# Kernel optimization log

Measured on AMD Instinct MI355X. Metric: run time of the kernel, lower is better.

## Reference

```python
import jax, jax.numpy as jnp
import numpy as np

N = 50000      # num nodes
E = 1600000    # num edges (before self-loops)
DIN, DH, DOUT = 256, 128, 64


def _gcn_norm(edge_index, num_nodes):
    # Add self-loops, then symmetric normalization 1/sqrt(deg_i * deg_j)
    loop = jnp.arange(num_nodes, dtype=edge_index.dtype)
    src = jnp.concatenate([edge_index[0], loop])  # [E+N]
    dst = jnp.concatenate([edge_index[1], loop])  # [E+N]
    deg = jax.ops.segment_sum(jnp.ones_like(dst, dtype=jnp.float32), dst,
                              num_segments=num_nodes)
    dinv = jnp.where(deg > 0, jax.lax.rsqrt(deg), 0.0)
    norm = dinv[src] * dinv[dst]  # [E+N]
    return src, dst, norm


def _gcn_conv(x, src, dst, norm, W, b, num_nodes):
    h = x @ W                                  # [N, out] dense transform first
    msg = h[src] * norm[:, None]               # gather + scale  [E+N, out]
    out = jax.ops.segment_sum(msg, dst, num_segments=num_nodes)  # scatter-add
    return out + b


def reference(x, edge_index, W1, b1, W2, b2):
    num_nodes = x.shape[0]
    src, dst, norm = _gcn_norm(edge_index, num_nodes)
    h = _gcn_conv(x, src, dst, norm, W1, b1, num_nodes)
    h = jax.nn.relu(h)
    # dropout(p=0.5) is identity in eval mode
    out = _gcn_conv(h, src, dst, norm, W2, b2, num_nodes)
    return out


def setup_inputs() -> dict:
    key = jax.random.key(0)
    ks = jax.random.split(key, 6)
    x = jax.random.normal(ks[0], (N, DIN), dtype=jnp.float32)
    edge_index = jax.random.randint(ks[1], (2, E), 0, N, dtype=jnp.int32)
    W1 = jax.random.normal(ks[2], (DIN, DH), dtype=jnp.float32) * (1.0 / np.sqrt(DIN))
    b1 = jnp.zeros((DH,), dtype=jnp.float32)
    W2 = jax.random.normal(ks[3], (DH, DOUT), dtype=jnp.float32) * (1.0 / np.sqrt(DH))
    b2 = jnp.zeros((DOUT,), dtype=jnp.float32)
    return {"x": x, "edge_index": edge_index, "W1": W1, "b1": b1, "W2": W2, "b2": b2}
```

## Files before the change

kernel.cpp:

```cpp
#include <hip/hip_runtime.h>

#define DIN 256
#define DH  128
#define DOUT 64
#define BSH  7
#define BNODES 128
#define MAXBUK 400
#define NBLK 512

typedef unsigned int  u32;
typedef unsigned short u16;
typedef __attribute__((ext_vector_type(8))) short bf16x8;
typedef __attribute__((ext_vector_type(4))) float f32x4;

__device__ inline u16 f2bf(float f) {
  u32 u = __float_as_uint(f);
  u32 r = u + 0x7FFF + ((u >> 16) & 1);
  return (u16)(r >> 16);
}
__device__ inline float bf2f_lo(u32 packed) { return __uint_as_float(packed << 16); }
__device__ inline float bf2f_hi(u32 packed) { return __uint_as_float(packed & 0xFFFF0000u); }


__global__ __launch_bounds__(256) void hist_kernel(const int* __restrict__ dst,
    int* __restrict__ counts, int E, int nbuk) {
  __shared__ int h[MAXBUK];
  int tid = threadIdx.x, b = blockIdx.x;
  for (int i = tid; i < nbuk; i += 256) h[i] = 0;
  __syncthreads();
  int ech = (E + NBLK - 1) / NBLK;
  int e0 = b * ech, e1 = min(E, e0 + ech);
  for (int e = e0 + tid; e < e1; e += 256)
    atomicAdd(&h[dst[e] >> BSH], 1);
  __syncthreads();
  for (int i = tid; i < nbuk; i += 256) counts[(size_t)i * NBLK + b] = h[i];
}

__global__ __launch_bounds__(256) void col_scan(int* __restrict__ counts,
    int* __restrict__ colsum, int nbuk) {
  __shared__ int sm[256];
  __shared__ int carry;
  int buk = blockIdx.x, t = threadIdx.x;
  if (t == 0) carry = 0;
  __syncthreads();
  int* row = counts + (size_t)buk * NBLK;
  for (int base = 0; base < NBLK; base += 256) {
    int v = row[base + t];
    sm[t] = v;
    __syncthreads();
    for (int d = 1; d < 256; d <<= 1) {
      int a = (t >= d) ? sm[t - d] : 0;
      __syncthreads();
      sm[t] += a;
      __syncthreads();
    }
    int excl = sm[t] - v + carry;
    row[base + t] = excl;
    __syncthreads();
    if (t == 255) carry = excl + v;
    __syncthreads();
  }
  if (t == 0) colsum[buk] = carry;
}

__global__ __launch_bounds__(256) void scan_block(int* partial, int* total_out, int nb, int n) {
  __shared__ int sm[256];
  __shared__ int carry;
  int t = threadIdx.x;
  if (t == 0) carry = 0;
  __syncthreads();
  for (int base = 0; base < nb; base += 256) {
    int g = base + t;
    int v = (g < nb) ? partial[g] : 0;
    sm[t] = v;
    __syncthreads();
    for (int d = 1; d < 256; d <<= 1) {
      int add = (t >= d) ? sm[t - d] : 0;
      __syncthreads();
      sm[t] += add;
      __syncthreads();
    }
    int excl = sm[t] - v + carry;
    if (g < nb) partial[g] = excl;
    __syncthreads();
    if (t == 255) carry = excl + v;
    __syncthreads();
  }
  if (t == 0) total_out[n] = carry;
}

__global__ __launch_bounds__(256) void scatter_kernel(const int* __restrict__ src,
    const int* __restrict__ dst, const int* __restrict__ counts,
    const int* __restrict__ bb, u32* __restrict__ ebuf, int E, int nbuk) {
  __shared__ int cur[MAXBUK];
  int tid = threadIdx.x, b = blockIdx.x;
  for (int i = tid; i < nbuk; i += 256)
    cur[i] = bb[i] + counts[(size_t)i * NBLK + b];
  __syncthreads();
  int ech = (E + NBLK - 1) / NBLK;
  int e0 = b * ech, e1 = min(E, e0 + ech);
  for (int e = e0 + tid; e < e1; e += 256) {
    int d = dst[e];
    int r = atomicAdd(&cur[d >> BSH], 1);
    ebuf[r] = (u32)src[e] | ((u32)(d & (BNODES - 1)) << 16);
  }
}

__global__ __launch_bounds__(256) void bucket_node_count(const u32* __restrict__ ebuf,
    const int* __restrict__ bb, int* __restrict__ cnt, int* __restrict__ bpartial, int N) {
  __shared__ int c[BNODES];
  int b = blockIdx.x, tid = threadIdx.x;
  if (tid < BNODES) c[tid] = 0;
  __syncthreads();
  int e0 = bb[b], e1 = bb[b + 1];
  for (int e = e0 + tid; e < e1; e += 256)
    atomicAdd(&c[ebuf[e] >> 16], 1);
  __syncthreads();
  int node = b * BNODES + tid;
  if (tid < BNODES && node < N) cnt[node] = c[tid];
  if (tid < 64) {
    int s = c[tid] + c[tid + 64];
    #pragma unroll
    for (int o = 32; o > 0; o >>= 1) s += __shfl_down(s, o, 64);
    if (tid == 0) bpartial[b] = s;
  }
}

__global__ __launch_bounds__(256) void scan_chunks(const int* __restrict__ cnt,
    const int* __restrict__ chunkoff, int* __restrict__ rowptr,
    float* __restrict__ dinv, int n) {
  __shared__ int sm[256];
  int t = threadIdx.x, g = blockIdx.x * 256 + t;
  int v = (g < n) ? cnt[g] : 0;
  sm[t] = v;
  __syncthreads();
  for (int d = 1; d < 256; d <<= 1) {
    int add = (t >= d) ? sm[t - d] : 0;
    __syncthreads();
    sm[t] += add;
    __syncthreads();
  }
  if (g < n) {
    rowptr[g] = sm[t] - v + chunkoff[blockIdx.x * 2];
    dinv[g] = rsqrtf((float)(v + 1));
  }
}

__global__ __launch_bounds__(256) void bucket_fill(const u32* __restrict__ ebuf,
    const int* __restrict__ bb, const int* __restrict__ rowptr, u16* __restrict__ csr) {
  __shared__ int c[BNODES];
  int b = blockIdx.x, tid = threadIdx.x;
  if (tid < BNODES) c[tid] = 0;
  __syncthreads();
  int e0 = bb[b], e1 = bb[b + 1];
  for (int e = e0 + tid; e < e1; e += 256) {
    u32 p = ebuf[e];
    int nl = p >> 16;
    int r = atomicAdd(&c[nl], 1);
    csr[rowptr[b * BNODES + nl] + r] = (u16)(p & 0xFFFFu);
  }
}


__global__ __launch_bounds__(256) void w_prep(const float* __restrict__ W1,
    const float* __restrict__ W2, u16* __restrict__ w1t, u32* __restrict__ w2p) {
  int t = blockIdx.x * 256 + threadIdx.x;
  if (t < DH * DIN) {
    int n = t >> 8, k = t & 255;
    w1t[t] = f2bf(W1[k * DH + n]);
  } else {
    int t2 = t - DH * DIN;
    int kk = t2 >> 6, j = t2 & 63;
    u32 lo = f2bf(W2[(2 * kk) * DOUT + j]);
    u32 hi = f2bf(W2[(2 * kk + 1) * DOUT + j]);
    w2p[t2] = lo | (hi << 16);
  }
}


__global__ __launch_bounds__(256) void gemm1_mfma(const float* __restrict__ x,
    const u16* __restrict__ w1t, const float* __restrict__ dinv,
    u16* __restrict__ h1, int M) {
  __shared__ u16 As[64][72];
  __shared__ u16 Bs[128][72];
  const int tid = threadIdx.x;
  const int lane = tid & 63, w = tid >> 6;
  const int row16 = lane & 15, quad = lane >> 4;
  const int rowBase = blockIdx.x * 64;
  f32x4 acc[8];
  #pragma unroll
  for (int nt = 0; nt < 8; ++nt) acc[nt] = (f32x4)(0.f);

  for (int kt = 0; kt < DIN; kt += 64) {
    {
      int r = tid >> 2, kq = tid & 3;
      int grow = rowBase + r;
      #pragma unroll
      for (int i = 0; i < 4; ++i) {
        float4 v = make_float4(0.f, 0.f, 0.f, 0.f);
        if (grow < M) v = *(const float4*)&x[(size_t)grow * DIN + kt + kq * 16 + i * 4];
        u32 lo = (u32)f2bf(v.x) | ((u32)f2bf(v.y) << 16);
        u32 hi = (u32)f2bf(v.z) | ((u32)f2bf(v.w) << 16);
        *(uint2*)&As[r][kq * 16 + i * 4] = make_uint2(lo, hi);
      }
    }
    {
      int n = tid >> 1, half = tid & 1;
      const uint4* s = (const uint4*)&w1t[n * DIN + kt + half * 32];
      uint4* d = (uint4*)&Bs[n][half * 32];
      d[0] = s[0]; d[1] = s[1]; d[2] = s[2]; d[3] = s[3];
    }
    __syncthreads();
    #pragma unroll
    for (int ks = 0; ks < 64; ks += 32) {
      bf16x8 a = *(bf16x8*)&As[w * 16 + row16][ks + quad * 8];
      #pragma unroll
      for (int nt = 0; nt < 8; ++nt) {
        bf16x8 b = *(bf16x8*)&Bs[nt * 16 + row16][ks + quad * 8];
        acc[nt] = __builtin_amdgcn_mfma_f32_16x16x32_bf16(a, b, acc[nt], 0, 0, 0);
      }
    }
    __syncthreads();
  }
  #pragma unroll
  for (int reg = 0; reg < 4; ++reg) {
    int row = rowBase + w * 16 + quad * 4 + reg;
    if (row < M) {
      float s = dinv[row];
      #pragma unroll
      for (int nt = 0; nt < 8; ++nt)
        h1[(size_t)row * DH + nt * 16 + row16] = f2bf(acc[nt][reg] * s);
    }
  }
}


__global__ __launch_bounds__(256) void aggregate1_fused(const u16* __restrict__ h,
    const int* __restrict__ rowptr, const u16* __restrict__ csr,
    const float* __restrict__ dinv, const float* __restrict__ bias,
    const u32* __restrict__ w2p, u16* __restrict__ h2, int n) {
  __shared__ u32 w2s[64 * 64];
  __shared__ float rowbuf[4][128];
  const int tid = threadIdx.x;
  {
    const uint4* s = (const uint4*)w2p;
    uint4* d = (uint4*)w2s;
    #pragma unroll
    for (int i = 0; i < 4; ++i) d[i * 256 + tid] = s[i * 256 + tid];
  }
  __syncthreads();

  const int lane = tid & 63;
  const int wv = tid >> 6;
  const int sub = lane >> 4;
  const int l16 = lane & 15;
  int node = blockIdx.x * 4 + wv;
  if (node >= n) return;
  node = __builtin_amdgcn_readfirstlane(node);
  const float di = dinv[node];
  const size_t coff = (size_t)l16 * 8;

  float a[8];
  {
    uint4 v = *(const uint4*)&h[(size_t)node * DH + coff];
    float ms = (sub == 0) ? 1.f : 0.f;
    a[0] = ms * bf2f_lo(v.x); a[1] = ms * bf2f_hi(v.x);
    a[2] = ms * bf2f_lo(v.y); a[3] = ms * bf2f_hi(v.y);
    a[4] = ms * bf2f_lo(v.z); a[5] = ms * bf2f_hi(v.z);
    a[6] = ms * bf2f_lo(v.w); a[7] = ms * bf2f_hi(v.w);
  }

  int p = rowptr[node];
  const int pe = rowptr[node + 1];
  while (p < pe) {
    int g = p + lane;
    int si = (g < pe) ? (int)csr[g] : 0;
    int rem = pe - p; if (rem > 64) rem = 64;
    int t = 0;
    for (; t + 16 <= rem; t += 16) {
      #pragma unroll
      for (int q = 0; q < 4; ++q) {
        int idx = __shfl(si, t + q * 4 + sub, 64);
        uint4 v = *(const uint4*)&h[(size_t)idx * DH + coff];
        a[0] += bf2f_lo(v.x); a[1] += bf2f_hi(v.x);
        a[2] += bf2f_lo(v.y); a[3] += bf2f_hi(v.y);
        a[4] += bf2f_lo(v.z); a[5] += bf2f_hi(v.z);
        a[6] += bf2f_lo(v.w); a[7] += bf2f_hi(v.w);
      }
    }
    for (; t < rem; t += 4) {
      int e = t + sub;
      int idx = __shfl(si, e & 63, 64);
      uint4 v = *(const uint4*)&h[(size_t)idx * DH + coff];
      float m = (e < rem) ? 1.f : 0.f;
      a[0] = fmaf(m, bf2f_lo(v.x), a[0]); a[1] = fmaf(m, bf2f_hi(v.x), a[1]);
      a[2] = fmaf(m, bf2f_lo(v.y), a[2]); a[3] = fmaf(m, bf2f_hi(v.y), a[3]);
      a[4] = fmaf(m, bf2f_lo(v.z), a[4]); a[5] = fmaf(m, bf2f_hi(v.z), a[5]);
      a[6] = fmaf(m, bf2f_lo(v.w), a[6]); a[7] = fmaf(m, bf2f_hi(v.w), a[7]);
    }
    p += 64;
  }

  #pragma unroll
  for (int i = 0; i < 8; ++i) {
    a[i] += __shfl_xor(a[i], 16, 64);
    a[i] += __shfl_xor(a[i], 32, 64);
  }

  const int c0 = l16 * 8;
  float4 b0 = *(const float4*)&bias[c0];
  float4 b1v = *(const float4*)&bias[c0 + 4];
  float f0 = fmaxf(fmaf(a[0], di, b0.x), 0.f);
  float f1 = fmaxf(fmaf(a[1], di, b0.y), 0.f);
  float f2 = fmaxf(fmaf(a[2], di, b0.z), 0.f);
  float f3 = fmaxf(fmaf(a[3], di, b0.w), 0.f);
  float f4 = fmaxf(fmaf(a[4], di, b1v.x), 0.f);
  float f5 = fmaxf(fmaf(a[5], di, b1v.y), 0.f);
  float f6 = fmaxf(fmaf(a[6], di, b1v.z), 0.f);
  float f7 = fmaxf(fmaf(a[7], di, b1v.w), 0.f);
  if (sub == 0) {
    float* rb = &rowbuf[wv][c0];
    rb[0] = f0; rb[1] = f1; rb[2] = f2; rb[3] = f3;
    rb[4] = f4; rb[5] = f5; rb[6] = f6; rb[7] = f7;
  }
  asm volatile("s_waitcnt lgkmcnt(0)" ::: "memory");
  __builtin_amdgcn_sched_barrier(0);

  const float* rb = rowbuf[wv];
  const u32* wrow = &w2s[lane];
  float o = 0.f;
  #pragma unroll
  for (int kk = 0; kk < 64; kk += 4) {
    float4 r01 = *(const float4*)&rb[2 * kk];
    float4 r23 = *(const float4*)&rb[2 * kk + 4];
    u32 w0 = wrow[(kk + 0) * 64];
    u32 w1 = wrow[(kk + 1) * 64];
    u32 w2v = wrow[(kk + 2) * 64];
    u32 w3 = wrow[(kk + 3) * 64];
    o = fmaf(r01.x, bf2f_lo(w0), o); o = fmaf(r01.y, bf2f_hi(w0), o);
    o = fmaf(r01.z, bf2f_lo(w1), o); o = fmaf(r01.w, bf2f_hi(w1), o);
    o = fmaf(r23.x, bf2f_lo(w2v), o); o = fmaf(r23.y, bf2f_hi(w2v), o);
    o = fmaf(r23.z, bf2f_lo(w3), o); o = fmaf(r23.w, bf2f_hi(w3), o);
  }
  o *= di;
  h2[(size_t)node * DOUT + lane] = f2bf(o);
}


__global__ __launch_bounds__(256) void aggregate2(const u16* __restrict__ h,
    const int* __restrict__ rowptr, const u16* __restrict__ csr,
    const float* __restrict__ dinv, const float* __restrict__ bias,
    float* __restrict__ out, int n) {
  const int lane = threadIdx.x & 63;
  const int sub = lane >> 3;
  const int l8 = lane & 7;
  int node = blockIdx.x * 4 + (threadIdx.x >> 6);
  if (node >= n) return;
  node = __builtin_amdgcn_readfirstlane(node);
  const float di = dinv[node];
  const size_t coff = (size_t)l8 * 8;

  float a[8];
  {
    uint4 v = *(const uint4*)&h[(size_t)node * DOUT + coff];
    float ms = (sub == 0) ? 1.f : 0.f;
    a[0] = ms * bf2f_lo(v.x); a[1] = ms * bf2f_hi(v.x);
    a[2] = ms * bf2f_lo(v.y); a[3] = ms * bf2f_hi(v.y);
    a[4] = ms * bf2f_lo(v.z); a[5] = ms * bf2f_hi(v.z);
    a[6] = ms * bf2f_lo(v.w); a[7] = ms * bf2f_hi(v.w);
  }

  int p = rowptr[node];
  const int pe = rowptr[node + 1];
  while (p < pe) {
    int g = p + lane;
    int si = (g < pe) ? (int)csr[g] : 0;
    int rem = pe - p; if (rem > 64) rem = 64;
    int t = 0;
    for (; t + 32 <= rem; t += 32) {
      #pragma unroll
      for (int q = 0; q < 4; ++q) {
        int idx = __shfl(si, t + q * 8 + sub, 64);
        uint4 v = *(const uint4*)&h[(size_t)idx * DOUT + coff];
        a[0] += bf2f_lo(v.x); a[1] += bf2f_hi(v.x);
        a[2] += bf2f_lo(v.y); a[3] += bf2f_hi(v.y);
        a[4] += bf2f_lo(v.z); a[5] += bf2f_hi(v.z);
        a[6] += bf2f_lo(v.w); a[7] += bf2f_hi(v.w);
      }
    }
    for (; t < rem; t += 8) {
      int e = t + sub;
      int idx = __shfl(si, e & 63, 64);
      uint4 v = *(const uint4*)&h[(size_t)idx * DOUT + coff];
      float m = (e < rem) ? 1.f : 0.f;
      a[0] = fmaf(m, bf2f_lo(v.x), a[0]); a[1] = fmaf(m, bf2f_hi(v.x), a[1]);
      a[2] = fmaf(m, bf2f_lo(v.y), a[2]); a[3] = fmaf(m, bf2f_hi(v.y), a[3]);
      a[4] = fmaf(m, bf2f_lo(v.z), a[4]); a[5] = fmaf(m, bf2f_hi(v.z), a[5]);
      a[6] = fmaf(m, bf2f_lo(v.w), a[6]); a[7] = fmaf(m, bf2f_hi(v.w), a[7]);
    }
    p += 64;
  }

  #pragma unroll
  for (int i = 0; i < 8; ++i) {
    a[i] += __shfl_xor(a[i], 8, 64);
    a[i] += __shfl_xor(a[i], 16, 64);
    a[i] += __shfl_xor(a[i], 32, 64);
  }

  if (sub == 0) {
    const int c0 = l8 * 8;
    float4 b0 = *(const float4*)&bias[c0];
    float4 b1 = *(const float4*)&bias[c0 + 4];
    float4 r0, r1;
    r0.x = fmaf(a[0], di, b0.x);
    r0.y = fmaf(a[1], di, b0.y);
    r0.z = fmaf(a[2], di, b0.z);
    r0.w = fmaf(a[3], di, b0.w);
    r1.x = fmaf(a[4], di, b1.x);
    r1.y = fmaf(a[5], di, b1.y);
    r1.z = fmaf(a[6], di, b1.z);
    r1.w = fmaf(a[7], di, b1.w);
    *(float4*)&out[(size_t)node * DOUT + c0] = r0;
    *(float4*)&out[(size_t)node * DOUT + c0 + 4] = r1;
  }
}


extern "C" void kernel_launch(void* const* d_in, const int* in_sizes, int n_in,
                              void* d_out, int out_size, void* d_ws, size_t ws_size,
                              hipStream_t stream) {
  const float* x  = (const float*)d_in[0];
  const int*   ei = (const int*)d_in[1];
  const float* W1 = (const float*)d_in[2];
  const float* b1 = (const float*)d_in[3];
  const float* W2 = (const float*)d_in[4];
  const float* b2 = (const float*)d_in[5];
  float* out = (float*)d_out;

  const int N = in_sizes[0] / DIN;
  const int E = in_sizes[1] / 2;
  const int* src = ei;
  const int* dst = ei + E;
  const int NB = (N + 255) / 256;
  const int nbuk = (N + BNODES - 1) / BNODES;

  char* ws = (char*)d_ws;
  size_t o = 0;
  auto alloc = [&](size_t bytes) { size_t r = o; o += (bytes + 511) & ~(size_t)511; return r; };
  size_t colsum_o  = alloc((size_t)(nbuk + 1) * 4);
  size_t counts_o  = alloc((size_t)nbuk * NBLK * 4);
  size_t rowptr_o  = alloc((size_t)(N + 1) * 4);
  size_t partial_o = alloc((size_t)(nbuk + 1) * 4);
  size_t dinv_o    = alloc((size_t)N * 4);
  size_t cnt_o     = alloc((size_t)N * 4);
  size_t w1t_o     = alloc((size_t)DH * DIN * 2);
  size_t w2p_o     = alloc((size_t)(DH / 2) * DOUT * 4);
  size_t csr_o     = alloc((size_t)E * 2);
  size_t h1_o      = alloc((size_t)N * DH * 2);
  size_t big_o     = alloc((size_t)E * 4);
  size_t h2_o      = big_o;

  int*   colsum  = (int*)(ws + colsum_o);
  int*   counts  = (int*)(ws + counts_o);
  int*   rowptr  = (int*)(ws + rowptr_o);
  int*   partial = (int*)(ws + partial_o);
  float* dinv    = (float*)(ws + dinv_o);
  int*   cnt     = (int*)(ws + cnt_o);
  u16*   w1t     = (u16*)(ws + w1t_o);
  u32*   w2p     = (u32*)(ws + w2p_o);
  u16*   csr     = (u16*)(ws + csr_o);
  u16*   h1      = (u16*)(ws + h1_o);
  u32*   ebuf    = (u32*)(ws + big_o);
  u16*   h2      = (u16*)(ws + h2_o);

  w_prep<<<(DH * DIN + (DH / 2) * DOUT) / 256, 256, 0, stream>>>(W1, W2, w1t, w2p);
  hist_kernel<<<NBLK, 256, 0, stream>>>(dst, counts, E, nbuk);
  col_scan<<<nbuk, 256, 0, stream>>>(counts, colsum, nbuk);
  scan_block<<<1, 256, 0, stream>>>(colsum, colsum, nbuk, nbuk);
  scatter_kernel<<<NBLK, 256, 0, stream>>>(src, dst, counts, colsum, ebuf, E, nbuk);
  bucket_node_count<<<nbuk, 256, 0, stream>>>(ebuf, colsum, cnt, partial, N);
  scan_block<<<1, 256, 0, stream>>>(partial, rowptr, nbuk, N);
  scan_chunks<<<NB, 256, 0, stream>>>(cnt, partial, rowptr, dinv, N);
  bucket_fill<<<nbuk, 256, 0, stream>>>(ebuf, colsum, rowptr, csr);

  gemm1_mfma<<<(N + 63) / 64, 256, 0, stream>>>(x, w1t, dinv, h1, N);
  aggregate1_fused<<<(N + 3) / 4, 256, 0, stream>>>(h1, rowptr, csr, dinv, b1, w2p, h2, N);
  aggregate2<<<(N + 3) / 4, 256, 0, stream>>>(h2, rowptr, csr, dinv, b2, out, N);
}
```

Measured before the change: 241.7 us.

## Use MFMA for fused second-layer transform in aggregate1 with bf16 row staging

Replaces the per-wave scalar FMA dot product (h1 row times W2) in the fused aggregation kernel with a block-wide 16x16x32 bf16 MFMA. The four node rows of a block are staged as bf16 in padded shared memory, with the remaining rows zeroed, and each wave computes 16 output columns. W2 is now pre-transposed to bf16 [DOUT][DH]. The cost is a block-level __syncthreads, 12 of 16 MFMA rows wasted on padding, and one extra bf16 rounding of the ReLU output. Inactive waves are kept alive instead of returning early so they can reach the barrier.

```diff
diff --git a/kernel.cpp b/kernel.cpp
--- a/kernel.cpp
+++ b/kernel.cpp
@@ -163,17 +163,15 @@
 
 
 __global__ __launch_bounds__(256) void w_prep(const float* __restrict__ W1,
-    const float* __restrict__ W2, u16* __restrict__ w1t, u32* __restrict__ w2p) {
+    const float* __restrict__ W2, u16* __restrict__ w1t, u16* __restrict__ w2t) {
   int t = blockIdx.x * 256 + threadIdx.x;
   if (t < DH * DIN) {
     int n = t >> 8, k = t & 255;
     w1t[t] = f2bf(W1[k * DH + n]);
   } else {
     int t2 = t - DH * DIN;
-    int kk = t2 >> 6, j = t2 & 63;
-    u32 lo = f2bf(W2[(2 * kk) * DOUT + j]);
-    u32 hi = f2bf(W2[(2 * kk + 1) * DOUT + j]);
-    w2p[t2] = lo | (hi << 16);
+    int j = t2 >> 7, k = t2 & 127;
+    w2t[t2] = f2bf(W2[k * DOUT + j]);
   }
 }
 
@@ -238,25 +236,33 @@
 __global__ __launch_bounds__(256) void aggregate1_fused(const u16* __restrict__ h,
     const int* __restrict__ rowptr, const u16* __restrict__ csr,
     const float* __restrict__ dinv, const float* __restrict__ bias,
-    const u32* __restrict__ w2p, u16* __restrict__ h2, int n) {
-  __shared__ u32 w2s[64 * 64];
-  __shared__ float rowbuf[4][128];
+    const u16* __restrict__ w2t, u16* __restrict__ h2, int n) {
+  __shared__ __align__(16) u16 w2s[64 * 136];
+  __shared__ __align__(16) u16 rowbuf[16 * 136];
   const int tid = threadIdx.x;
-  {
-    const uint4* s = (const uint4*)w2p;
-    uint4* d = (uint4*)w2s;
-    #pragma unroll
-    for (int i = 0; i < 4; ++i) d[i * 256 + tid] = s[i * 256 + tid];
-  }
-  __syncthreads();
-
   const int lane = tid & 63;
   const int wv = tid >> 6;
-  const int sub = lane >> 4;
-  const int l16 = lane & 15;
-  int node = blockIdx.x * 4 + wv;
-  if (node >= n) return;
-  node = __builtin_amdgcn_readfirstlane(node);
+  const int row16 = lane & 15, quad = lane >> 4;
+
+  {
+    #pragma unroll
+    for (int i = 0; i < 4; ++i) {
+      int flat = i * 256 + tid;
+      int r = flat >> 4, q = flat & 15;
+      *(uint4*)&w2s[r * 136 + q * 8] = *(const uint4*)&w2t[r * 128 + q * 8];
+    }
+  }
+  if (wv < 3) {
+    int r = 4 + wv * 4 + quad;
+    *(uint4*)&rowbuf[r * 136 + row16 * 8] = make_uint4(0, 0, 0, 0);
+  }
+
+  const int sub = quad;
+  const int l16 = row16;
+  const int nodeBase = blockIdx.x * 4;
+  int node = nodeBase + wv;
+  const bool active = node < n;
+  node = __builtin_amdgcn_readfirstlane(active ? node : (n - 1));
   const float di = dinv[node];
   const size_t coff = (size_t)l16 * 8;
 
@@ -271,7 +277,7 @@
   }
 
   int p = rowptr[node];
-  const int pe = rowptr[node + 1];
+  const int pe = active ? rowptr[node + 1] : p;
   while (p < pe) {
     int g = p + lane;
     int si = (g < pe) ? (int)csr[g] : 0;
@@ -307,43 +313,42 @@
     a[i] += __shfl_xor(a[i], 32, 64);
   }
 
-  const int c0 = l16 * 8;
-  float4 b0 = *(const float4*)&bias[c0];
-  float4 b1v = *(const float4*)&bias[c0 + 4];
-  float f0 = fmaxf(fmaf(a[0], di, b0.x), 0.f);
-  float f1 = fmaxf(fmaf(a[1], di, b0.y), 0.f);
-  float f2 = fmaxf(fmaf(a[2], di, b0.z), 0.f);
-  float f3 = fmaxf(fmaf(a[3], di, b0.w), 0.f);
-  float f4 = fmaxf(fmaf(a[4], di, b1v.x), 0.f);
-  float f5 = fmaxf(fmaf(a[5], di, b1v.y), 0.f);
-  float f6 = fmaxf(fmaf(a[6], di, b1v.z), 0.f);
-  float f7 = fmaxf(fmaf(a[7], di, b1v.w), 0.f);
   if (sub == 0) {
-    float* rb = &rowbuf[wv][c0];
-    rb[0] = f0; rb[1] = f1; rb[2] = f2; rb[3] = f3;
-    rb[4] = f4; rb[5] = f5; rb[6] = f6; rb[7] = f7;
-  }
-  asm volatile("s_waitcnt lgkmcnt(0)" ::: "memory");
-  __builtin_amdgcn_sched_barrier(0);
-
-  const float* rb = rowbuf[wv];
-  const u32* wrow = &w2s[lane];
-  float o = 0.f;
+    const int c0 = l16 * 8;
+    float4 b0 = *(const float4*)&bias[c0];
+    float4 b1v = *(const float4*)&bias[c0 + 4];
+    float f0 = fmaxf(fmaf(a[0], di, b0.x), 0.f);
+    float f1 = fmaxf(fmaf(a[1], di, b0.y), 0.f);
+    float f2 = fmaxf(fmaf(a[2], di, b0.z), 0.f);
+    float f3 = fmaxf(fmaf(a[3], di, b0.w), 0.f);
+    float f4 = fmaxf(fmaf(a[4], di, b1v.x), 0.f);
+    float f5 = fmaxf(fmaf(a[5], di, b1v.y), 0.f);
+    float f6 = fmaxf(fmaf(a[6], di, b1v.z), 0.f);
+    float f7 = fmaxf(fmaf(a[7], di, b1v.w), 0.f);
+    uint4 pk;
+    pk.x = (u32)f2bf(f0) | ((u32)f2bf(f1) << 16);
+    pk.y = (u32)f2bf(f2) | ((u32)f2bf(f3) << 16);
+    pk.z = (u32)f2bf(f4) | ((u32)f2bf(f5) << 16);
+    pk.w = (u32)f2bf(f6) | ((u32)f2bf(f7) << 16);
+    *(uint4*)&rowbuf[wv * 136 + l16 * 8] = pk;
+  }
+  __syncthreads();
+
+  f32x4 acc = (f32x4)(0.f);
   #pragma unroll
-  for (int kk = 0; kk < 64; kk += 4) {
-    float4 r01 = *(const float4*)&rb[2 * kk];
-    float4 r23 = *(const float4*)&rb[2 * kk + 4];
-    u32 w0 = wrow[(kk + 0) * 64];
-    u32 w1 = wrow[(kk + 1) * 64];
-    u32 w2v = wrow[(kk + 2) * 64];
-    u32 w3 = wrow[(kk + 3) * 64];
-    o = fmaf(r01.x, bf2f_lo(w0), o); o = fmaf(r01.y, bf2f_hi(w0), o);
-    o = fmaf(r01.z, bf2f_lo(w1), o); o = fmaf(r01.w, bf2f_hi(w1), o);
-    o = fmaf(r23.x, bf2f_lo(w2v), o); o = fmaf(r23.y, bf2f_hi(w2v), o);
-    o = fmaf(r23.z, bf2f_lo(w3), o); o = fmaf(r23.w, bf2f_hi(w3), o);
-  }
-  o *= di;
-  h2[(size_t)node * DOUT + lane] = f2bf(o);
+  for (int kt = 0; kt < 4; ++kt) {
+    bf16x8 af = *(bf16x8*)&rowbuf[row16 * 136 + kt * 32 + quad * 8];
+    bf16x8 bf = *(bf16x8*)&w2s[(wv * 16 + row16) * 136 + kt * 32 + quad * 8];
+    acc = __builtin_amdgcn_mfma_f32_16x16x32_bf16(af, bf, acc, 0, 0, 0);
+  }
+  if (quad == 0) {
+    #pragma unroll
+    for (int reg = 0; reg < 4; ++reg) {
+      int nr = nodeBase + reg;
+      if (nr < n)
+        h2[(size_t)nr * DOUT + wv * 16 + row16] = f2bf(acc[reg] * dinv[nr]);
+    }
+  }
 }
 
 
@@ -455,7 +460,7 @@
   size_t dinv_o    = alloc((size_t)N * 4);
   size_t cnt_o     = alloc((size_t)N * 4);
   size_t w1t_o     = alloc((size_t)DH * DIN * 2);
-  size_t w2p_o     = alloc((size_t)(DH / 2) * DOUT * 4);
+  size_t w2t_o     = alloc((size_t)DOUT * DH * 2);
   size_t csr_o     = alloc((size_t)E * 2);
   size_t h1_o      = alloc((size_t)N * DH * 2);
   size_t big_o     = alloc((size_t)E * 4);
@@ -468,13 +473,13 @@
   float* dinv    = (float*)(ws + dinv_o);
   int*   cnt     = (int*)(ws + cnt_o);
   u16*   w1t     = (u16*)(ws + w1t_o);
-  u32*   w2p     = (u32*)(ws + w2p_o);
+  u16*   w2t     = (u16*)(ws + w2t_o);
   u16*   csr     = (u16*)(ws + csr_o);
   u16*   h1      = (u16*)(ws + h1_o);
   u32*   ebuf    = (u32*)(ws + big_o);
   u16*   h2      = (u16*)(ws + h2_o);
 
-  w_prep<<<(DH * DIN + (DH / 2) * DOUT) / 256, 256, 0, stream>>>(W1, W2, w1t, w2p);
+  w_prep<<<(DH * DIN + DOUT * DH) / 256, 256, 0, stream>>>(W1, W2, w1t, w2t);
   hist_kernel<<<NBLK, 256, 0, stream>>>(dst, counts, E, nbuk);
   col_scan<<<nbuk, 256, 0, stream>>>(counts, colsum, nbuk);
   scan_block<<<1, 256, 0, stream>>>(colsum, colsum, nbuk, nbuk);
@@ -485,6 +490,6 @@
   bucket_fill<<<nbuk, 256, 0, stream>>>(ebuf, colsum, rowptr, csr);
 
   gemm1_mfma<<<(N + 63) / 64, 256, 0, stream>>>(x, w1t, dinv, h1, N);
-  aggregate1_fused<<<(N + 3) / 4, 256, 0, stream>>>(h1, rowptr, csr, dinv, b1, w2p, h2, N);
+  aggregate1_fused<<<(N + 3) / 4, 256, 0, stream>>>(h1, rowptr, csr, dinv, b1, w2t, h2, N);
   aggregate2<<<(N + 3) / 4, 256, 0, stream>>>(h2, rowptr, csr, dinv, b2, out, N);
 }
```

Result: no change. 240.0 us (-0.7%).
